# Performance work log

Measured on AMD Instinct MI355X. Metric: run time of the kernel, lower is better.

The kernel has to match this reference:

```python
import jax, jax.numpy as jnp
import numpy as np

BIT_WIDTH = 8
UP = float(2 ** (BIT_WIDTH - 1) - 1)   # 127
LOW = float(-(2 ** (BIT_WIDTH - 1)))   # -128


def setup_inputs() -> dict:
    key = jax.random.key(0)
    k1, k2, k3, k4, k5 = jax.random.split(key, 5)
    B, Cin, H, W = 32, 256, 56, 56
    Cout, kH, kW = 256, 3, 3
    x = jax.random.normal(k1, (B, Cin, H, W), dtype=jnp.float32)
    weight = jax.random.normal(k2, (Cout, Cin, kH, kW), dtype=jnp.float32) * 0.05
    bias = jax.random.normal(k3, (Cout,), dtype=jnp.float32) * 0.1
    # positive quantization scales (roughly map |w|~0.15, |x|~3 into int8 range)
    sw = jax.random.uniform(k4, (Cout,), minval=200.0, maxval=800.0, dtype=jnp.float32)
    sx = jax.random.uniform(k5, (1,), minval=20.0, maxval=40.0, dtype=jnp.float32)
    return {"x": x, "weight": weight, "bias": bias, "sw": sw, "sx": sx}


def reference(x, weight, bias, sw, sx):
    """QConv2d forward in q_inference (quant-simulation) mode:
    per-out-channel fake-quantize weight, per-tensor fake-quantize input,
    then float conv2d + bias. jnp.round matches torch.round (half-to-even)."""
    swb = sw[:, None, None, None]                      # [Cout,1,1,1]
    q_w = jnp.round(jnp.clip(weight * swb, LOW, UP)) / swb
    q_x = jnp.round(jnp.clip(x * sx[0], LOW, UP)) / sx[0]
    out = jax.lax.conv_general_dilated(
        q_x, q_w,
        window_strides=(1, 1),
        padding=((1, 1), (1, 1)),
        dimension_numbers=("NCHW", "OIHW", "NCHW"),
    )
    return out + bias[None, :, None, None]
```

## Files before the change

### kernel.cpp

```cpp
#include <hip/hip_runtime.h>
#include <stdint.h>

typedef int int32x4 __attribute__((ext_vector_type(4)));

#define HW_        3136
#define CHW_       802816
#define HP_        58
#define WP_        58
#define PLANE_PIX  107648ull
#define PLANE_B    (PLANE_PIX*16)
#define QXP_BYTES  (16ull*PLANE_B)
#define QWT_BYTES  (9ull*16*256*16)

__device__ __forceinline__ signed char quant8(float v, float s) {
    float t = v * s;
    t = fmaxf(t, -128.0f);
    t = fminf(t, 127.0f);
    return (signed char)(int)rintf(t);
}

__global__ __launch_bounds__(256) void prep_kernel(
    const float* __restrict__ x, const float* __restrict__ sx,
    const float* __restrict__ wgt, const float* __restrict__ sw,
    signed char* __restrict__ qxp2, signed char* __restrict__ qwT2)
{
    __shared__ __align__(16) signed char lw[9*272];
    const int tid = threadIdx.x;
    const int blk = blockIdx.x;

    if (blk >= 1792) {
        const int o = blk - 1792;
        const float s = sw[o];
        const float* wp = wgt + ((size_t)o*256 + tid)*9;
        #pragma unroll
        for (int kk = 0; kk < 9; ++kk)
            lw[kk*272 + tid] = quant8(wp[kk], s);
        __syncthreads();
        if (tid < 144) {
            int kk = tid / 16, cq = tid - kk*16;
            int32x4 v = *(const int32x4*)&lw[kk*272 + cq*16];
            *(int32x4*)(qwT2 + ((size_t)(kk*16 + cq)*256 + o)*16) = v;
        }
        return;
    }

    const int b = blk / 56, h = blk % 56;
    const float s = sx[0];
    if (tid < 224) {
        const int w  = tid % 56;
        const int cg = tid / 56;
        const size_t xrow = (size_t)b*CHW_ + (size_t)h*56 + w;
        const size_t pb = ((size_t)(b*HP_ + h + 1)*WP_ + 1 + w)*16;
        #pragma unroll
        for (int k = 0; k < 4; ++k) {
            const int cq = cg*4 + k;
            const float* xp = x + xrow + (size_t)(cq*16)*HW_;
            int pk[4];
            #pragma unroll
            for (int g = 0; g < 4; ++g) {
                int b0 = (unsigned char)quant8(xp[(size_t)(4*g+0)*HW_], s);
                int b1 = (unsigned char)quant8(xp[(size_t)(4*g+1)*HW_], s);
                int b2 = (unsigned char)quant8(xp[(size_t)(4*g+2)*HW_], s);
                int b3 = (unsigned char)quant8(xp[(size_t)(4*g+3)*HW_], s);
                pk[g] = b0 | (b1 << 8) | (b2 << 16) | (b3 << 24);
            }
            *(int32x4*)(qxp2 + (size_t)cq*PLANE_B + pb) = (int32x4){pk[0],pk[1],pk[2],pk[3]};
        }
    } else {
        int t2 = tid - 224;
        int cq = t2 >> 1, wp = (t2 & 1) * (WP_-1);
        const size_t rowpix = (size_t)(b*HP_ + h + 1)*WP_;
        *(int32x4*)(qxp2 + ((size_t)cq*PLANE_PIX + rowpix + wp)*16) = (int32x4){0,0,0,0};
    }
    if (h == 0) {
        for (int t = tid; t < 16*2*58; t += 256) {
            int cq = t / 116;
            int r  = t - cq*116;
            int hp = (r / 58) * (HP_-1);
            int wp = r % 58;
            *(int32x4*)(qxp2 + ((size_t)cq*PLANE_PIX + (size_t)(b*HP_+hp)*WP_ + wp)*16)
                = (int32x4){0,0,0,0};
        }
    }
}

__device__ __forceinline__ void load16_lds(const void* g, void* l) {
    __builtin_amdgcn_global_load_lds(
        (const unsigned int*)g,
        reinterpret_cast<__attribute__((address_space(3))) unsigned int*>(
            reinterpret_cast<uintptr_t>(l)),
        16, 0, 0);
}

#define LOADA4(st, AF) {                                                      \
    const signed char* aG_ = qwT2 + (size_t)(((st) >> 2)*65536                \
                           + (((st) & 3)*4)*4096) + aRow;                     \
    AF[0] = *(const int32x4*)(aG_ +   0);                                     \
    AF[1] = *(const int32x4*)(aG_ + 256);                                     \
    AF[2] = *(const int32x4*)(aG_ + 512);                                     \
    AF[3] = *(const int32x4*)(aG_ + 768);                                     \
}

#define STAGEB(st) {                                                          \
    const size_t ksh_ = (size_t)((((st) >> 2)/3)*WP_ + (((st) >> 2)%3))*16;   \
    const signed char* bG_ = qxp2 + (size_t)(((st) & 3)*4)*PLANE_B            \
                           + wOffB + ksh_;                                    \
    signed char* dst_ = smem + ((st)%3)*8192 + dstW;                          \
    load16_lds(bG_ + bOff0, dst_);                                            \
    load16_lds(bG_ + bOff1, dst_ + 1024);                                     \
}

#define STEP(st, AC, AN) {                                                    \
    if ((st) == 35) asm volatile("s_waitcnt vmcnt(4)");                       \
    else            asm volatile("s_waitcnt vmcnt(6)");                       \
    __builtin_amdgcn_s_barrier();                                             \
    __builtin_amdgcn_sched_barrier(0);                                        \
    if ((st) + 1 < 36) LOADA4((st) + 1, AN);                                  \
    if ((st) + 2 < 36) STAGEB((st) + 2);                                      \
    const signed char* bR_ = smem + ((st)%3)*8192;                            \
    int32x4 bf[4];                                                            \
    _Pragma("unroll")                                                         \
    for (int t = 0; t < 4; ++t)                                               \
        bf[t] = *(const int32x4*)&bR_[rdOff + t*256];                         \
    __builtin_amdgcn_s_setprio(1);                                            \
    _Pragma("unroll")                                                         \
    for (int mt = 0; mt < 4; ++mt)                                            \
        _Pragma("unroll")                                                     \
        for (int nt = 0; nt < 4; ++nt)                                        \
            acc[mt][nt] = __builtin_amdgcn_mfma_i32_16x16x64_i8(              \
                AC[mt], bf[nt], acc[mt][nt], 0, 0, 0);                        \
    __builtin_amdgcn_s_setprio(0);                                            \
    __builtin_amdgcn_sched_barrier(0);                                        \
}

#define STEP2(s) STEP((s),   aP, aQ) STEP((s)+1, aQ, aP)
#define STEP6(s) STEP2(s) STEP2((s)+2) STEP2((s)+4)

__global__ __launch_bounds__(256, 3) void conv_kernel(
    const signed char* __restrict__ qxp2, const signed char* __restrict__ qwT2,
    const float* __restrict__ sw, const float* __restrict__ bias,
    const float* __restrict__ sx, float* __restrict__ out)
{
    __shared__ __align__(16) signed char smem[34816];

    const int tid  = threadIdx.x;
    const int wv   = tid >> 6;
    const int lane = tid & 63;
    const int quad = lane >> 4;
    const int l15  = lane & 15;

    const int bid = blockIdx.x;
    const int swz = (bid & 7) * 196 + (bid >> 3);
    const int s0  = (swz >> 1) * 128;
    const int o0  = (swz & 1) * 128;

    const unsigned sp0 = (unsigned)(s0 + lane);
    const unsigned sp1 = (unsigned)(s0 + 64 + lane);
    unsigned b0 = sp0 / HW_, r0 = sp0 - b0*HW_;
    unsigned b1 = sp1 / HW_, r1 = sp1 - b1*HW_;
    unsigned h0 = r0 / 56,   w0 = r0 - h0*56;
    unsigned h1 = r1 / 56,   w1 = r1 - h1*56;
    const size_t bOff0 = ((size_t)(b0*HP_ + h0)*WP_ + w0)*16;
    const size_t bOff1 = ((size_t)(b1*HP_ + h1)*WP_ + w1)*16;

    const int wo = (wv & 1) << 6;
    const int wn = (wv >> 1) << 6;
    const size_t aRow  = (size_t)quad*4096 + (size_t)(o0 + wo + l15)*16;
    const size_t wOffB = (size_t)wv*PLANE_B;
    const int    dstW  = wv*2048;
    const int    rdOff = quad*2048 + (wn + l15)*16;

    int32x4 acc[4][4];
    #pragma unroll
    for (int i = 0; i < 4; ++i)
        #pragma unroll
        for (int j = 0; j < 4; ++j)
            acc[i][j] = (int32x4){0,0,0,0};

    int32x4 aP[4], aQ[4];

    STAGEB(0);
    STAGEB(1);
    __builtin_amdgcn_sched_barrier(0);
    LOADA4(0, aP);
    __builtin_amdgcn_sched_barrier(0);

    STEP6(0) STEP6(6) STEP6(12) STEP6(18) STEP6(24) STEP6(30)

    asm volatile("" ::: "memory");

    float* lt    = (float*)smem;
    float* invS  = (float*)(smem + 33792);
    float* biasS = (float*)(smem + 34304);
    if (tid < 128) {
        float s = sw[o0 + tid];
        invS[tid]  = 1.0f / (s * sx[0]);
        biasS[tid] = bias[o0 + tid];
    }
    #pragma unroll
    for (int p = 0; p < 2; ++p) {
        __syncthreads();
        if ((wv & 1) == p) {
            #pragma unroll
            for (int mt = 0; mt < 4; ++mt)
                #pragma unroll
                for (int nt = 0; nt < 4; ++nt)
                    #pragma unroll
                    for (int r = 0; r < 4; ++r)
                        lt[(mt*16 + quad*4 + r)*132 + wn + nt*16 + l15]
                            = (float)acc[mt][nt][r];
        }
        __syncthreads();
        #pragma unroll
        for (int i = 0; i < 8; ++i) {
            int idx = i*256 + tid;
            int o = idx >> 5;
            int c = idx & 31;
            float4 v = *(const float4*)&lt[o*132 + 4*c];
            int ol = p*64 + o;
            float is = invS[ol], bs = biasS[ol];
            unsigned sp = (unsigned)(s0 + 4*c);
            unsigned b  = sp / HW_;
            unsigned pos = sp - b*HW_;
            float4 wv4;
            wv4.x = fmaf(v.x, is, bs); wv4.y = fmaf(v.y, is, bs);
            wv4.z = fmaf(v.z, is, bs); wv4.w = fmaf(v.w, is, bs);
            *(float4*)(out + (size_t)b*CHW_ + (size_t)(o0 + ol)*HW_ + pos) = wv4;
        }
    }
}

extern "C" void kernel_launch(void* const* d_in, const int* in_sizes, int n_in,
                              void* d_out, int out_size, void* d_ws, size_t ws_size,
                              hipStream_t stream)
{
    (void)in_sizes; (void)n_in; (void)out_size; (void)ws_size;
    const float* x    = (const float*)d_in[0];
    const float* wgt  = (const float*)d_in[1];
    const float* bias = (const float*)d_in[2];
    const float* sw   = (const float*)d_in[3];
    const float* sx   = (const float*)d_in[4];
    float* out = (float*)d_out;

    signed char* qxp2 = (signed char*)d_ws;
    signed char* qwT2 = qxp2 + QXP_BYTES;

    prep_kernel<<<2048, 256, 0, stream>>>(x, sx, wgt, sw, qxp2, qwT2);
    conv_kernel<<<1568, 256, 0, stream>>>(qxp2, qwT2, sw, bias, sx, out);
}
```

Before: 263.9 us.

## Stage contiguous halo row once and reuse it across the three kw taps

The B-operand staging now copies one contiguous padded input strip (128 pixels plus halo) per kh row and channel group into LDS. The three kw taps then read from that strip at shifted offsets, instead of doing a separate global-to-LDS load for each of the 36 (tap, channel-group) steps. This cuts global/L2 traffic for the input and the barrier count by about 3x, and the main loop becomes 12 stages of 3 taps each. In exchange, LDS use grows to 48 KB, which may limit occupancy at 3 blocks per CU. Per-lane LDS read offsets are also irregular across batch and row boundaries, which risks bank conflicts.

```diff
diff --git a/kernel.cpp b/kernel.cpp
--- a/kernel.cpp
+++ b/kernel.cpp
@@ -92,36 +92,32 @@
         16, 0, 0);
 }
 
-#define LOADA4(st, AF) {                                                      \
-    const signed char* aG_ = qwT2 + (size_t)(((st) >> 2)*65536                \
-                           + (((st) & 3)*4)*4096) + aRow;                     \
+#define STAGEB(st) {                                                          \
+    const signed char* bG_ = qxp2                                             \
+        + (size_t)(((st) & 3)*4 + wv)*PLANE_B                                 \
+        + (base0 + (size_t)((st) >> 2)*WP_)*16 + (size_t)lane*16;             \
+    signed char* dst_ = smem + ((st)%3)*16384 + wv*4096;                      \
+    load16_lds(bG_ +    0, dst_ +    0);                                      \
+    load16_lds(bG_ + 1024, dst_ + 1024);                                      \
+    load16_lds(bG_ + 2048, dst_ + 2048);                                      \
+    load16_lds(bG_ + 3072, dst_ + 3072);                                      \
+}
+
+#define LOADA(nst, nkw, AF) {                                                 \
+    const signed char* aG_ = aBase + (size_t)((((nst) >> 2)*3 + (nkw))*65536  \
+                           + ((nst) & 3)*16384);                              \
     AF[0] = *(const int32x4*)(aG_ +   0);                                     \
     AF[1] = *(const int32x4*)(aG_ + 256);                                     \
     AF[2] = *(const int32x4*)(aG_ + 512);                                     \
     AF[3] = *(const int32x4*)(aG_ + 768);                                     \
 }
 
-#define STAGEB(st) {                                                          \
-    const size_t ksh_ = (size_t)((((st) >> 2)/3)*WP_ + (((st) >> 2)%3))*16;   \
-    const signed char* bG_ = qxp2 + (size_t)(((st) & 3)*4)*PLANE_B            \
-                           + wOffB + ksh_;                                    \
-    signed char* dst_ = smem + ((st)%3)*8192 + dstW;                          \
-    load16_lds(bG_ + bOff0, dst_);                                            \
-    load16_lds(bG_ + bOff1, dst_ + 1024);                                     \
-}
-
-#define STEP(st, AC, AN) {                                                    \
-    if ((st) == 35) asm volatile("s_waitcnt vmcnt(4)");                       \
-    else            asm volatile("s_waitcnt vmcnt(6)");                       \
-    __builtin_amdgcn_s_barrier();                                             \
-    __builtin_amdgcn_sched_barrier(0);                                        \
-    if ((st) + 1 < 36) LOADA4((st) + 1, AN);                                  \
-    if ((st) + 2 < 36) STAGEB((st) + 2);                                      \
-    const signed char* bR_ = smem + ((st)%3)*8192;                            \
+#define TAP(st, kw, AC, AN, nst, nkw) {                                       \
+    if ((nst) < 12) LOADA(nst, nkw, AN);                                      \
     int32x4 bf[4];                                                            \
     _Pragma("unroll")                                                         \
     for (int t = 0; t < 4; ++t)                                               \
-        bf[t] = *(const int32x4*)&bR_[rdOff + t*256];                         \
+        bf[t] = *(const int32x4*)&smem[rA[t] + ((st)%3)*16384 + (kw)*16];     \
     __builtin_amdgcn_s_setprio(1);                                            \
     _Pragma("unroll")                                                         \
     for (int mt = 0; mt < 4; ++mt)                                            \
@@ -133,15 +129,22 @@
     __builtin_amdgcn_sched_barrier(0);                                        \
 }
 
-#define STEP2(s) STEP((s),   aP, aQ) STEP((s)+1, aQ, aP)
-#define STEP6(s) STEP2(s) STEP2((s)+2) STEP2((s)+4)
+#define SS(st, X, Y) {                                                        \
+    asm volatile("s_waitcnt vmcnt(8)");                                       \
+    __builtin_amdgcn_s_barrier();                                             \
+    __builtin_amdgcn_sched_barrier(0);                                        \
+    if ((st) + 2 < 12) STAGEB((st) + 2);                                      \
+    TAP(st, 0, X, Y, st, 1)                                                   \
+    TAP(st, 1, Y, X, st, 2)                                                   \
+    TAP(st, 2, X, Y, (st) + 1, 0)                                             \
+}
 
 __global__ __launch_bounds__(256, 3) void conv_kernel(
     const signed char* __restrict__ qxp2, const signed char* __restrict__ qwT2,
     const float* __restrict__ sw, const float* __restrict__ bias,
     const float* __restrict__ sx, float* __restrict__ out)
 {
-    __shared__ __align__(16) signed char smem[34816];
+    __shared__ __align__(16) signed char smem[49152];
 
     const int tid  = threadIdx.x;
     const int wv   = tid >> 6;
@@ -154,21 +157,25 @@
     const int s0  = (swz >> 1) * 128;
     const int o0  = (swz & 1) * 128;
 
-    const unsigned sp0 = (unsigned)(s0 + lane);
-    const unsigned sp1 = (unsigned)(s0 + 64 + lane);
-    unsigned b0 = sp0 / HW_, r0 = sp0 - b0*HW_;
-    unsigned b1 = sp1 / HW_, r1 = sp1 - b1*HW_;
-    unsigned h0 = r0 / 56,   w0 = r0 - h0*56;
-    unsigned h1 = r1 / 56,   w1 = r1 - h1*56;
-    const size_t bOff0 = ((size_t)(b0*HP_ + h0)*WP_ + w0)*16;
-    const size_t bOff1 = ((size_t)(b1*HP_ + h1)*WP_ + w1)*16;
-
     const int wo = (wv & 1) << 6;
     const int wn = (wv >> 1) << 6;
-    const size_t aRow  = (size_t)quad*4096 + (size_t)(o0 + wo + l15)*16;
-    const size_t wOffB = (size_t)wv*PLANE_B;
-    const int    dstW  = wv*2048;
-    const int    rdOff = quad*2048 + (wn + l15)*16;
+
+    const unsigned tb = (unsigned)s0 / HW_;
+    const unsigned ttr = (unsigned)s0 - tb*HW_;
+    const unsigned th = ttr / 56, twc = ttr - th*56;
+    const size_t base0 = (size_t)(tb*HP_ + th)*WP_ + twc;
+
+    int rA[4];
+    #pragma unroll
+    for (int t = 0; t < 4; ++t) {
+        unsigned sp = (unsigned)(s0 + wn + t*16 + l15);
+        unsigned b = sp / HW_, r = sp - b*HW_;
+        unsigned h = r / 56,   w = r - h*56;
+        unsigned slot = (b*HP_ + h)*WP_ + w;
+        rA[t] = quad*4096 + (int)(slot - (unsigned)base0)*16;
+    }
+
+    const signed char* aBase = qwT2 + (size_t)quad*4096 + (size_t)(o0 + wo + l15)*16;
 
     int32x4 acc[4][4];
     #pragma unroll
@@ -182,12 +189,14 @@
     STAGEB(0);
     STAGEB(1);
     __builtin_amdgcn_sched_barrier(0);
-    LOADA4(0, aP);
+    LOADA(0, 0, aP);
     __builtin_amdgcn_sched_barrier(0);
 
-    STEP6(0) STEP6(6) STEP6(12) STEP6(18) STEP6(24) STEP6(30)
-
-    asm volatile("" ::: "memory");
+    SS(0,  aP, aQ)  SS(1,  aQ, aP)  SS(2,  aP, aQ)  SS(3,  aQ, aP)
+    SS(4,  aP, aQ)  SS(5,  aQ, aP)  SS(6,  aP, aQ)  SS(7,  aQ, aP)
+    SS(8,  aP, aQ)  SS(9,  aQ, aP)  SS(10, aP, aQ)  SS(11, aQ, aP)
+
+    __syncthreads();
 
     float* lt    = (float*)smem;
     float* invS  = (float*)(smem + 33792);
```

After: 249.9 us. 5.3% less time.
